# Kernel tuning notes

Measured on AMD Instinct MI355X. Metric: run time of the kernel, lower is better.

The kernel has to match this reference:

```python
import jax, jax.numpy as jnp
import numpy as np


def setup_inputs() -> dict:
    key = jax.random.key(0)
    T, B, I, M = 256, 64, 512, 512
    ks = jax.random.split(key, 16)
    kai_i = np.sqrt(2.0 / I)   # kaiming_normal_ fan_in
    kai_m = np.sqrt(2.0 / M)
    return {
        "inputs":   jax.random.normal(ks[0], (T, B, I), jnp.float32),
        "sememe_c": jax.random.normal(ks[1], (T, B, M), jnp.float32),
        "sememe_h": jax.random.normal(ks[2], (T, B, M), jnp.float32),
        "c0":       jax.random.normal(ks[3], (B, M), jnp.float32),
        "h0":       jax.random.normal(ks[4], (B, M), jnp.float32),
        "W_ioux": jax.random.normal(ks[5], (3 * M, I), jnp.float32) * kai_i,
        "b_ioux": jnp.zeros((3 * M,), jnp.float32),
        "W_iouh": jax.random.normal(ks[6], (3 * M, M), jnp.float32) * kai_m,
        "b_iouh": jnp.zeros((3 * M,), jnp.float32),
        "W_ious": jax.random.normal(ks[7], (3 * M, M), jnp.float32) * kai_m,
        "b_ious": jnp.zeros((3 * M,), jnp.float32),
        "W_fx":  jax.random.normal(ks[8],  (M, I), jnp.float32) * kai_i,
        "b_fx":  jnp.zeros((M,), jnp.float32),
        "W_fxs": jax.random.normal(ks[9],  (M, I), jnp.float32) * kai_i,
        "b_fxs": jnp.zeros((M,), jnp.float32),
        "W_fh":  jax.random.normal(ks[10], (M, M), jnp.float32) * kai_m,
        "b_fh":  jnp.zeros((M,), jnp.float32),
        "W_fs":  jax.random.normal(ks[11], (M, M), jnp.float32) * kai_m,
        "b_fs":  jnp.zeros((M,), jnp.float32),
    }


def reference(inputs, sememe_c, sememe_h, c0, h0,
              W_ioux, b_ioux, W_iouh, b_iouh, W_ious, b_ious,
              W_fx, b_fx, W_fxs, b_fxs, W_fh, b_fh, W_fs, b_fs):
    # Precompute all input-side projections with big GEMMs over [T*B, I].
    iou_x = jnp.einsum('tbi,oi->tbo', inputs, W_ioux) + b_ioux   # [T,B,3M]
    fx_all = jnp.einsum('tbi,oi->tbo', inputs, W_fx) + b_fx       # [T,B,M]
    fxs_all = jnp.einsum('tbi,oi->tbo', inputs, W_fxs) + b_fxs    # [T,B,M]

    def step(carry, xs):
        c, h = carry
        iou_x_t, fx_t, fxs_t, sc_t, sh_t = xs
        iou = iou_x_t + h @ W_iouh.T + b_iouh + sh_t @ W_ious.T + b_ious
        i, o, u = jnp.split(iou, 3, axis=1)
        i = jax.nn.sigmoid(i)
        o = jax.nn.sigmoid(o)
        u = jnp.tanh(u)
        f = jax.nn.sigmoid(h @ W_fh.T + b_fh + fx_t)
        f_s = jax.nn.sigmoid(sh_t @ W_fs.T + b_fs + fxs_t)
        c_new = i * u + f * c + f_s * sc_t
        h_new = o * jnp.tanh(c_new)
        return (c_new, h_new), h_new

    (c_T, h_T), output = jax.lax.scan(
        step, (c0, h0), (iou_x, fx_all, fxs_all, sememe_c, sememe_h))
    return output, c_T, h_T
```

## Files before the change

kernel.cpp:

```cpp
#include <hip/hip_runtime.h>
#include <cstdint>
#include <cstddef>


typedef _Float16 half8 __attribute__((ext_vector_type(8)));
typedef _Float16 half4 __attribute__((ext_vector_type(4)));
typedef float    f32x4 __attribute__((ext_vector_type(4)));
typedef unsigned int uint32x4 __attribute__((ext_vector_type(4)));

#define T_STEPS 256
#define B_DIM   64
#define M_DIM   512
#define KA      1024
#define NA      2560
#define MA      16384
#define NWG_REC 64
#define FLAG_STRIDE 32

__device__ __forceinline__ float sigmoidf_fast(float x) {
    return 1.0f / (1.0f + __expf(-x));
}
__device__ __forceinline__ float tanhf_fast(float x) {
    float e = __expf(2.0f * x);
    return 1.0f - 2.0f / (e + 1.0f);
}
__device__ __forceinline__ void wg_barrier() {
    asm volatile("" ::: "memory");
    __builtin_amdgcn_s_barrier();
    asm volatile("" ::: "memory");
}


__global__ void conv_xs(const float* __restrict__ inp, const float* __restrict__ sh,
                        _Float16* __restrict__ xs) {
    int idx = blockIdx.x * blockDim.x + threadIdx.x;
    const int total = MA * KA / 8;
    if (idx >= total) return;
    int row = idx >> 7;
    int col = (idx & 127) * 8;
    const float* src = (col < 512) ? (inp + (size_t)row * 512 + col)
                                   : (sh  + (size_t)row * 512 + (col - 512));
    f32x4 a = *(const f32x4*)src;
    f32x4 b = *(const f32x4*)(src + 4);
    half8 o;
    o[0]=(_Float16)a[0]; o[1]=(_Float16)a[1]; o[2]=(_Float16)a[2]; o[3]=(_Float16)a[3];
    o[4]=(_Float16)b[0]; o[5]=(_Float16)b[1]; o[6]=(_Float16)b[2]; o[7]=(_Float16)b[3];
    *(half8*)(xs + (size_t)idx * 8) = o;
}

__global__ void conv_w(const float* __restrict__ W_ioux, const float* __restrict__ W_ious,
                       const float* __restrict__ W_fx,   const float* __restrict__ W_fxs,
                       const float* __restrict__ W_fs,   _Float16* __restrict__ wc) {
    int idx = blockIdx.x * blockDim.x + threadIdx.x;
    const int total = NA * KA / 8;
    if (idx >= total) return;
    int n = idx >> 7;
    int col = (idx & 127) * 8;
    const float* src = nullptr;
    if (col < 512) {
        int k = col;
        src = (n < 1536) ? (W_ioux + (size_t)n * 512 + k)
            : (n < 2048) ? (W_fx   + (size_t)(n - 1536) * 512 + k)
                         : (W_fxs  + (size_t)(n - 2048) * 512 + k);
    } else {
        int k = col - 512;
        if (n < 1536)      src = W_ious + (size_t)n * 512 + k;
        else if (n >= 2048) src = W_fs  + (size_t)(n - 2048) * 512 + k;
    }
    half8 o;
    if (src) {
        f32x4 a = *(const f32x4*)src;
        f32x4 b = *(const f32x4*)(src + 4);
        o[0]=(_Float16)a[0]; o[1]=(_Float16)a[1]; o[2]=(_Float16)a[2]; o[3]=(_Float16)a[3];
        o[4]=(_Float16)b[0]; o[5]=(_Float16)b[1]; o[6]=(_Float16)b[2]; o[7]=(_Float16)b[3];
    } else {
        #pragma unroll
        for (int i = 0; i < 8; ++i) o[i] = (_Float16)0.0f;
    }
    *(half8*)(wc + (size_t)idx * 8) = o;
}

__global__ void conv_wr(const float* __restrict__ W_iouh, const float* __restrict__ W_fh,
                        _Float16* __restrict__ wr) {
    int idx = blockIdx.x * blockDim.x + threadIdx.x;
    const int total = 2048 * 512 / 8;
    if (idx >= total) return;
    int n = idx >> 6;
    int col = (idx & 63) * 8;
    int wgs = n >> 5, loc = n & 31;
    int g = (loc >> 4) * 2 + ((loc >> 3) & 1);
    int m = wgs * 8 + (loc & 7);
    const float* src = (g < 3) ? (W_iouh + ((size_t)(g * 512 + m)) * 512 + col)
                               : (W_fh   + (size_t)m * 512 + col);
    f32x4 a = *(const f32x4*)src;
    f32x4 b = *(const f32x4*)(src + 4);
    half8 o;
    o[0]=(_Float16)a[0]; o[1]=(_Float16)a[1]; o[2]=(_Float16)a[2]; o[3]=(_Float16)a[3];
    o[4]=(_Float16)b[0]; o[5]=(_Float16)b[1]; o[6]=(_Float16)b[2]; o[7]=(_Float16)b[3];
    *(half8*)(wr + (size_t)idx * 8) = o;
}

__global__ void conv_h0(const float* __restrict__ h0, unsigned short* __restrict__ hb) {
    int idx = blockIdx.x * blockDim.x + threadIdx.x;
    const int total = B_DIM * M_DIM / 8;
    if (idx >= total) return;
    f32x4 a = *(const f32x4*)(h0 + (size_t)idx * 8);
    f32x4 b = *(const f32x4*)(h0 + (size_t)idx * 8 + 4);
    unsigned short o[8];
    #pragma unroll
    for (int j = 0; j < 4; ++j) {
        _Float16 ha = (_Float16)a[j], hbv = (_Float16)b[j];
        o[j]     = (unsigned short)(__builtin_bit_cast(unsigned short, ha)  & 0xFFFCu);
        o[j + 4] = (unsigned short)(__builtin_bit_cast(unsigned short, hbv) & 0xFFFCu);
    }
    uint32x4 pk;
    pk[0] = o[0] | ((unsigned)o[1] << 16);
    pk[1] = o[2] | ((unsigned)o[3] << 16);
    pk[2] = o[4] | ((unsigned)o[5] << 16);
    pk[3] = o[6] | ((unsigned)o[7] << 16);
    *(uint32x4*)(hb + (size_t)idx * 8) = pk;
}


__global__ __launch_bounds__(256, 2)
void gemm_pre(const _Float16* __restrict__ A, const _Float16* __restrict__ W,
              const float* __restrict__ b_ioux, const float* __restrict__ b_iouh,
              const float* __restrict__ b_ious, const float* __restrict__ b_fx,
              const float* __restrict__ b_fh,   const float* __restrict__ b_fxs,
              const float* __restrict__ b_fs,   const float* __restrict__ smc,
              _Float16* __restrict__ pre, _Float16* __restrict__ addc) {
    __shared__ _Float16 As[128 * 64];
    __shared__ _Float16 Bs[128 * 64];

    const int nwg = 2560;
    int orig = blockIdx.x;
    int wgid = (orig & 7) * (nwg >> 3) + (orig >> 3);
    const int bx = wgid & 127;
    const int by = wgid >> 7;
    const int m0 = bx * 128, n0 = by * 128;

    const int tid = threadIdx.x;
    const int wv = tid >> 6, lane = tid & 63;
    const int lr = lane & 15, lq = lane >> 4;
    const int wr = wv >> 1, wc = wv & 1;

    f32x4 acc[4][4];
    #pragma unroll
    for (int i = 0; i < 4; ++i)
        #pragma unroll
        for (int j = 0; j < 4; ++j)
            #pragma unroll
            for (int r = 0; r < 4; ++r) acc[i][j][r] = 0.0f;

    for (int kt = 0; kt < KA / 64; ++kt) {
        const int k0 = kt * 64;
        #pragma unroll
        for (int j = 0; j < 4; ++j) {
            int L = j * 4096 + wv * 1024 + lane * 16;
            int row = L >> 7;
            int colb = (L & 127) ^ ((row & 7) << 4);
            const char* ga = (const char*)(A + (size_t)(m0 + row) * KA + k0) + colb;
            __builtin_amdgcn_global_load_lds(
                (const __attribute__((address_space(1))) void*)ga,
                (__attribute__((address_space(3))) void*)((char*)As + j * 4096 + wv * 1024),
                16, 0, 0);
            const char* gb = (const char*)(W + (size_t)(n0 + row) * KA + k0) + colb;
            __builtin_amdgcn_global_load_lds(
                (const __attribute__((address_space(1))) void*)gb,
                (__attribute__((address_space(3))) void*)((char*)Bs + j * 4096 + wv * 1024),
                16, 0, 0);
        }
        __syncthreads();

        half8 af[4][2], bf[4][2];
        #pragma unroll
        for (int f = 0; f < 4; ++f) {
            #pragma unroll
            for (int kk = 0; kk < 2; ++kk) {
                {
                    int row = wr * 64 + f * 16 + lr;
                    int byt = row * 128 + (((kk * 32 + lq * 8) * 2) ^ ((row & 7) << 4));
                    af[f][kk] = *(const half8*)((const char*)As + byt);
                }
                {
                    int row = wc * 64 + f * 16 + lr;
                    int byt = row * 128 + (((kk * 32 + lq * 8) * 2) ^ ((row & 7) << 4));
                    bf[f][kk] = *(const half8*)((const char*)Bs + byt);
                }
            }
        }
        #pragma unroll
        for (int kk = 0; kk < 2; ++kk)
            #pragma unroll
            for (int fi = 0; fi < 4; ++fi)
                #pragma unroll
                for (int fj = 0; fj < 4; ++fj)
                    acc[fi][fj] = __builtin_amdgcn_mfma_f32_16x16x32_f16(
                        af[fi][kk], bf[fj][kk], acc[fi][fj], 0, 0, 0);
        __syncthreads();
    }

    #pragma unroll
    for (int fi = 0; fi < 4; ++fi) {
        int row0 = m0 + wr * 64 + fi * 16 + lq * 4;
        int tt = row0 >> 6;
        int b  = row0 & 63;
        #pragma unroll
        for (int fj = 0; fj < 4; ++fj) {
            int col = n0 + wc * 64 + fj * 16 + lr;
            f32x4 v = acc[fi][fj];
            if (col < 2048) {
                int g, mm; float bias;
                if (col < 1536) { g = col >> 9; mm = col & 511;
                                  bias = b_ioux[col] + b_iouh[col] + b_ious[col]; }
                else            { g = 3; mm = col - 1536; bias = b_fx[mm] + b_fh[mm]; }
                half4 hv;
                #pragma unroll
                for (int r = 0; r < 4; ++r) hv[r] = (_Float16)(v[r] + bias);
                *(half4*)(pre + ((((size_t)tt * 4 + g) * 512 + mm) * 64 + b)) = hv;
            } else {
                int mm = col - 2048;
                float bias = b_fxs[mm] + b_fs[mm];
                half4 hv;
                #pragma unroll
                for (int r = 0; r < 4; ++r) {
                    float s  = sigmoidf_fast(v[r] + bias);
                    float sc = smc[((size_t)(tt * 64 + b + r)) * 512 + mm];
                    hv[r] = (_Float16)(s * sc);
                }
                *(half4*)(addc + (((size_t)tt * 512 + mm) * 64 + b)) = hv;
            }
        }
    }
}


__device__ __forceinline__ bool gather_try8(const char* bp, unsigned pat,
                                            half8 (&af)[8]) {
    asm volatile(
        "global_load_dwordx4 %0, %8, off sc0 sc1\n\t"
        "global_load_dwordx4 %1, %8, off offset:64 sc0 sc1\n\t"
        "global_load_dwordx4 %2, %8, off offset:128 sc0 sc1\n\t"
        "global_load_dwordx4 %3, %8, off offset:192 sc0 sc1\n\t"
        "global_load_dwordx4 %4, %8, off offset:256 sc0 sc1\n\t"
        "global_load_dwordx4 %5, %8, off offset:320 sc0 sc1\n\t"
        "global_load_dwordx4 %6, %8, off offset:384 sc0 sc1\n\t"
        "global_load_dwordx4 %7, %8, off offset:448 sc0 sc1\n\t"
        "s_waitcnt vmcnt(0)"
        : "=&v"(af[0]), "=&v"(af[1]), "=&v"(af[2]), "=&v"(af[3]),
          "=&v"(af[4]), "=&v"(af[5]), "=&v"(af[6]), "=&v"(af[7])
        : "v"(bp)
        : "memory");
    unsigned bad = 0;
    #pragma unroll
    for (int j = 0; j < 8; ++j) {
        uint32x4 dv = __builtin_bit_cast(uint32x4, af[j]);
        #pragma unroll
        for (int d = 0; d < 4; ++d) bad |= (dv[d] & 0x00030003u) ^ pat;
    }
    return __all(bad == 0);
}

template<int G>
__device__ __forceinline__ void lstm_phase(
    int t, int wg, int mi, int ki, int lane, int lq, int lr, int c8, int m,
    const half8 (&bfr)[2][8], float (&c)[4],
    const _Float16* __restrict__ pre, const _Float16* __restrict__ addc,
    unsigned short* __restrict__ hbuf, float* __restrict__ out,
    int* __restrict__ flags, f32x4 (*red)[64][2]) {

    const int rb = G * 32 + mi * 16;
    const int b0 = rb + lq * 4;

    half4 pv[2], av;
    if (ki == 0) {
        #pragma unroll
        for (int nt = 0; nt < 2; ++nt) {
            int g = nt * 2 + c8;
            pv[nt] = *(const half4*)(pre + (((size_t)t * 4 + g) * 512 + m) * 64 + b0);
        }
        av = *(const half4*)(addc + ((size_t)t * 512 + m) * 64 + b0);
    }

    const char* bp = (const char*)hbuf + (size_t)(t & 1) * 65536
                     + ((size_t)(rb + lr) * 512 + ki * 256 + lq * 8) * 2;
    const unsigned pat = (unsigned)(t & 3) * 0x00010001u;
    half8 af[8];
    if (!gather_try8(bp, pat, af)) {
        const int* fp = flags + ((size_t)G * 64 + lane) * FLAG_STRIDE;
        while (true) {
            int v;
            asm volatile("global_load_dword %0, %1, off sc0 sc1\n\t"
                         "s_waitcnt vmcnt(0)"
                         : "=v"(v) : "v"(fp) : "memory");
            if (__all(v >= t)) break;
            __builtin_amdgcn_s_sleep(1);
        }
        while (!gather_try8(bp, pat, af))
            __builtin_amdgcn_s_sleep(1);
    }

    f32x4 acc[2];
    if (ki == 0) {
        #pragma unroll
        for (int nt = 0; nt < 2; ++nt)
            #pragma unroll
            for (int r = 0; r < 4; ++r) acc[nt][r] = (float)pv[nt][r];
    } else {
        #pragma unroll
        for (int nt = 0; nt < 2; ++nt)
            #pragma unroll
            for (int r = 0; r < 4; ++r) acc[nt][r] = 0.0f;
    }
    #pragma unroll
    for (int kk = 0; kk < 8; ++kk) {
        acc[0] = __builtin_amdgcn_mfma_f32_16x16x32_f16(af[kk], bfr[0][kk], acc[0], 0, 0, 0);
        acc[1] = __builtin_amdgcn_mfma_f32_16x16x32_f16(af[kk], bfr[1][kk], acc[1], 0, 0, 0);
    }

    wg_barrier();
    if (ki == 1) {
        red[mi][lane][0] = acc[0];
        red[mi][lane][1] = acc[1];
    }
    asm volatile("s_waitcnt lgkmcnt(0)" ::: "memory");
    wg_barrier();

    if (ki == 0) {
        f32x4 p0 = red[mi][lane][0], p1 = red[mi][lane][1];
        #pragma unroll
        for (int r = 0; r < 4; ++r) { acc[0][r] += p0[r]; acc[1][r] += p1[r]; }

        float hnew[4];
        #pragma unroll
        for (int r = 0; r < 4; ++r) {
            float raw0 = acc[0][r];
            float raw1 = acc[1][r];
            float s0 = sigmoidf_fast(raw0);
            float v1 = c8 ? sigmoidf_fast(raw1) : tanhf_fast(raw1);
            float sf = __shfl_xor(v1, 8);
            float cn = s0 * v1 + sf * c[r] + (float)av[r];
            float tc = tanhf_fast(cn);
            float tcx = __shfl_xor(tc, 8);
            if (!c8) c[r] = cn;
            hnew[r] = s0 * tcx;
        }

        if (t < T_STEPS - 1) {
            unsigned short* hw = hbuf + (size_t)((t + 1) & 1) * 32768;
            const unsigned tag1 = (unsigned)((t + 1) & 3);
            if (c8) {
                #pragma unroll
                for (int r = 0; r < 4; ++r) {
                    _Float16 hv = (_Float16)hnew[r];
                    unsigned u = ((unsigned)__builtin_bit_cast(unsigned short, hv)
                                  & 0xFFFCu) | tag1;
                    asm volatile("global_store_short %0, %1, off sc0 sc1"
                                 :: "v"(hw + (size_t)(b0 + r) * 512 + m), "v"(u)
                                 : "memory");
                }
            }
            if (mi == 0 && lane == 0) {
                unsigned fv = (unsigned)(t + 1);
                asm volatile("global_store_dword %0, %1, off sc0 sc1"
                             :: "v"(flags + ((size_t)G * 64 + wg) * FLAG_STRIDE),
                                "v"(fv) : "memory");
            }
            if (c8) {
                #pragma unroll
                for (int r = 0; r < 4; ++r)
                    out[((size_t)t * B_DIM + b0 + r) * M_DIM + m] = hnew[r];
            }
        } else {
            if (c8) {
                #pragma unroll
                for (int r = 0; r < 4; ++r)
                    out[((size_t)t * B_DIM + b0 + r) * M_DIM + m] = hnew[r];
            }
            size_t base = (size_t)T_STEPS * B_DIM * M_DIM;
            if (!c8) {
                #pragma unroll
                for (int r = 0; r < 4; ++r)
                    out[base + (size_t)(b0 + r) * M_DIM + m] = c[r];
            } else {
                #pragma unroll
                for (int r = 0; r < 4; ++r)
                    out[base + (size_t)B_DIM * M_DIM + (size_t)(b0 + r) * M_DIM + m] = hnew[r];
            }
        }
    }
}

__global__ __launch_bounds__(256, 1)
void lstm_rec(const _Float16* __restrict__ Wr, const _Float16* __restrict__ pre,
              const _Float16* __restrict__ addc, const float* __restrict__ c0,
              unsigned short* __restrict__ hbuf, float* __restrict__ out,
              int* __restrict__ flags) {
    __shared__ f32x4 red[2][64][2];

    const int wg = blockIdx.x;
    const int tid = threadIdx.x;
    const int wv = tid >> 6, lane = tid & 63;
    const int mi = wv >> 1, ki = wv & 1;
    const int lr = lane & 15, lq = lane >> 4;
    const int c8 = (lane >> 3) & 1;
    const int m  = wg * 8 + (lane & 7);

    half8 bfr[2][8];
    #pragma unroll
    for (int nt = 0; nt < 2; ++nt)
        #pragma unroll
        for (int kk = 0; kk < 8; ++kk)
            bfr[nt][kk] = *(const half8*)(Wr + ((size_t)(wg * 32 + nt * 16 + lr)) * 512
                                          + ki * 256 + kk * 32 + lq * 8);

    float cA[4], cB[4];
    {
        int b0A = 0  + mi * 16 + lq * 4;
        int b0B = 32 + mi * 16 + lq * 4;
        #pragma unroll
        for (int r = 0; r < 4; ++r) {
            cA[r] = c0[(size_t)(b0A + r) * 512 + m];
            cB[r] = c0[(size_t)(b0B + r) * 512 + m];
        }
    }

    for (int t = 0; t < T_STEPS; ++t) {
        lstm_phase<0>(t, wg, mi, ki, lane, lq, lr, c8, m, bfr, cA,
                      pre, addc, hbuf, out, flags, red);
        lstm_phase<1>(t, wg, mi, ki, lane, lq, lr, c8, m, bfr, cB,
                      pre, addc, hbuf, out, flags, red);
    }
}


extern "C" void kernel_launch(void* const* d_in, const int* in_sizes, int n_in,
                              void* d_out, int out_size, void* d_ws, size_t ws_size,
                              hipStream_t stream) {
    const float* inputs  = (const float*)d_in[0];
    const float* smc     = (const float*)d_in[1];
    const float* smh     = (const float*)d_in[2];
    const float* c0      = (const float*)d_in[3];
    const float* h0      = (const float*)d_in[4];
    const float* W_ioux  = (const float*)d_in[5];
    const float* b_ioux  = (const float*)d_in[6];
    const float* W_iouh  = (const float*)d_in[7];
    const float* b_iouh  = (const float*)d_in[8];
    const float* W_ious  = (const float*)d_in[9];
    const float* b_ious  = (const float*)d_in[10];
    const float* W_fx    = (const float*)d_in[11];
    const float* b_fx    = (const float*)d_in[12];
    const float* W_fxs   = (const float*)d_in[13];
    const float* b_fxs   = (const float*)d_in[14];
    const float* W_fh    = (const float*)d_in[15];
    const float* b_fh    = (const float*)d_in[16];
    const float* W_fs    = (const float*)d_in[17];
    const float* b_fs    = (const float*)d_in[18];

    char* ws = (char*)d_ws;
    size_t off = 0;
    auto alloc = [&](size_t bytes) {
        char* p = ws + off;
        off = (off + bytes + 255) & ~(size_t)255;
        return p;
    };
    _Float16* XS   = (_Float16*)alloc((size_t)MA * KA * 2);
    _Float16* Wc   = (_Float16*)alloc((size_t)NA * KA * 2);
    _Float16* Wr   = (_Float16*)alloc((size_t)2048 * 512 * 2);
    unsigned short* hb = (unsigned short*)alloc((size_t)2 * B_DIM * M_DIM * 2);
    _Float16* pre  = (_Float16*)alloc((size_t)T_STEPS * 4 * 512 * 64 * 2);
    _Float16* addc = (_Float16*)alloc((size_t)T_STEPS * 512 * 64 * 2);
    int* flags     = (int*)alloc((size_t)2 * NWG_REC * FLAG_STRIDE * sizeof(int));
    if (off > ws_size) return;

    hipMemsetAsync(flags, 0, (size_t)2 * NWG_REC * FLAG_STRIDE * sizeof(int), stream);
    conv_xs <<<MA * KA / 8 / 256, 256, 0, stream>>>(inputs, smh, XS);
    conv_w  <<<NA * KA / 8 / 256, 256, 0, stream>>>(W_ioux, W_ious, W_fx, W_fxs, W_fs, Wc);
    conv_wr <<<2048 * 512 / 8 / 256, 256, 0, stream>>>(W_iouh, W_fh, Wr);
    conv_h0 <<<B_DIM * M_DIM / 8 / 256, 256, 0, stream>>>(h0, hb);
    gemm_pre<<<2560, 256, 0, stream>>>(XS, Wc, b_ioux, b_iouh, b_ious, b_fx, b_fh,
                                       b_fxs, b_fs, smc, pre, addc);
    lstm_rec<<<NWG_REC, 256, 0, stream>>>(Wr, pre, addc, c0, hb, (float*)d_out, flags);
}
```

Before: 1.522 ms.

## Prefetch next phase's hidden-state tile into LDS with async global_load_lds

Each wave now issues asynchronous global-to-LDS loads of the hidden-state slice for the next phase (the other batch half) before doing the current phase's math. At phase start it waits on outstanding memory ops, reads the staged tile from LDS, and checks the step-parity tag bits. It falls back to the old flag-polling global gather if the prefetched data was stale. The goal is to hide global gather latency on the recurrent critical path. The risk is that the data is often not yet published when prefetched, so the fallback runs anyway. It also adds 64KB of LDS and a full vmcnt wait that also covers pending output stores.

```diff
diff --git a/kernel.cpp b/kernel.cpp
--- a/kernel.cpp
+++ b/kernel.cpp
@@ -261,32 +261,52 @@
     return __all(bad == 0);
 }
 
+__device__ __forceinline__ void issue_stage(
+    const unsigned short* __restrict__ hbuf, char* lds_wave_base,
+    int G, int t, int mi, int ki, int lr, int lq) {
+    const char* src0 = (const char*)hbuf + (size_t)(t & 1) * 65536
+        + ((size_t)(G * 32 + mi * 16 + lr) * 512 + ki * 256 + lq * 8) * 2;
+    #pragma unroll
+    for (int j = 0; j < 8; ++j)
+        __builtin_amdgcn_global_load_lds(
+            (const __attribute__((address_space(1))) void*)(src0 + j * 64),
+            (__attribute__((address_space(3))) void*)(lds_wave_base + j * 1024),
+            16, 0, 17);
+}
+
 template<int G>
 __device__ __forceinline__ void lstm_phase(
     int t, int wg, int mi, int ki, int lane, int lq, int lr, int c8, int m,
     const half8 (&bfr)[2][8], float (&c)[4],
     const _Float16* __restrict__ pre, const _Float16* __restrict__ addc,
     unsigned short* __restrict__ hbuf, float* __restrict__ out,
-    int* __restrict__ flags, f32x4 (*red)[64][2]) {
+    int* __restrict__ flags, f32x4 (*red)[64][2], char* hstage) {
 
     const int rb = G * 32 + mi * 16;
     const int b0 = rb + lq * 4;
-
-    half4 pv[2], av;
-    if (ki == 0) {
-        #pragma unroll
-        for (int nt = 0; nt < 2; ++nt) {
-            int g = nt * 2 + c8;
-            pv[nt] = *(const half4*)(pre + (((size_t)t * 4 + g) * 512 + m) * 64 + b0);
-        }
-        av = *(const half4*)(addc + ((size_t)t * 512 + m) * 64 + b0);
-    }
-
-    const char* bp = (const char*)hbuf + (size_t)(t & 1) * 65536
-                     + ((size_t)(rb + lr) * 512 + ki * 256 + lq * 8) * 2;
+    const int wv = mi * 2 + ki;
+    char* myStage = hstage + (size_t)G * 32768 + (size_t)wv * 8192;
+
+    asm volatile("s_waitcnt vmcnt(0)" ::: "memory");
+
+    half8 af[8];
+    {
+        const char* lb = myStage + lane * 16;
+        #pragma unroll
+        for (int j = 0; j < 8; ++j)
+            af[j] = *(const half8*)(lb + j * 1024);
+    }
     const unsigned pat = (unsigned)(t & 3) * 0x00010001u;
-    half8 af[8];
-    if (!gather_try8(bp, pat, af)) {
+    unsigned bad = 0;
+    #pragma unroll
+    for (int j = 0; j < 8; ++j) {
+        uint32x4 dv = __builtin_bit_cast(uint32x4, af[j]);
+        #pragma unroll
+        for (int d = 0; d < 4; ++d) bad |= (dv[d] & 0x00030003u) ^ pat;
+    }
+    if (!__all(bad == 0)) {
+        const char* bp = (const char*)hbuf + (size_t)(t & 1) * 65536
+                       + ((size_t)(rb + lr) * 512 + ki * 256 + lq * 8) * 2;
         const int* fp = flags + ((size_t)G * 64 + lane) * FLAG_STRIDE;
         while (true) {
             int v;
@@ -298,6 +318,24 @@
         }
         while (!gather_try8(bp, pat, af))
             __builtin_amdgcn_s_sleep(1);
+    }
+
+    {
+        const int tn = t + G;
+        if (tn < T_STEPS) {
+            char* nStage = hstage + (size_t)(G ^ 1) * 32768 + (size_t)wv * 8192;
+            issue_stage(hbuf, nStage, G ^ 1, tn, mi, ki, lr, lq);
+        }
+    }
+
+    half4 pv[2], av;
+    if (ki == 0) {
+        #pragma unroll
+        for (int nt = 0; nt < 2; ++nt) {
+            int g = nt * 2 + c8;
+            pv[nt] = *(const half4*)(pre + (((size_t)t * 4 + g) * 512 + m) * 64 + b0);
+        }
+        av = *(const half4*)(addc + ((size_t)t * 512 + m) * 64 + b0);
     }
 
     f32x4 acc[2];
@@ -397,6 +435,7 @@
               unsigned short* __restrict__ hbuf, float* __restrict__ out,
               int* __restrict__ flags) {
     __shared__ f32x4 red[2][64][2];
+    __shared__ __align__(1024) char hstage[2][32768];
 
     const int wg = blockIdx.x;
     const int tid = threadIdx.x;
@@ -425,11 +464,13 @@
         }
     }
 
+    issue_stage(hbuf, &hstage[0][0] + (size_t)wv * 8192, 0, 0, mi, ki, lr, lq);
+
     for (int t = 0; t < T_STEPS; ++t) {
         lstm_phase<0>(t, wg, mi, ki, lane, lq, lr, c8, m, bfr, cA,
-                      pre, addc, hbuf, out, flags, red);
+                      pre, addc, hbuf, out, flags, red, &hstage[0][0]);
         lstm_phase<1>(t, wg, mi, ki, lane, lq, lr, c8, m, bfr, cB,
-                      pre, addc, hbuf, out, flags, red);
+                      pre, addc, hbuf, out, flags, red, &hstage[0][0]);
     }
 }
 
```

Result: slower. 1.880 ms (+23.5%).
